# Kernel tuning notes

Measured on AMD Instinct MI355X. Metric: run time of the kernel, lower is better.

The kernel has to match this reference:

```python
import jax, jax.numpy as jnp
import numpy as np

B, OBS, ACT, NT, E, H1, H2, D = 4096, 390, 20, 10, 8, 1024, 512, 256


def setup_inputs() -> dict:
    key = jax.random.key(0)
    ks = jax.random.split(key, 16)
    f32 = jnp.float32

    def w(k, shape, fan_in):
        return jax.random.normal(k, shape, f32) / np.float32(np.sqrt(fan_in))

    return {
        "state_feat": jax.random.normal(ks[0], (B, OBS), f32),
        "act": jax.random.normal(ks[1], (B, ACT), f32),
        "task_id": jax.random.randint(ks[2], (B,), 0, NT, jnp.int32),
        "rep_W1": w(ks[3], (OBS + ACT, H1), OBS + ACT),
        "rep_b1": jnp.zeros((H1,), f32),
        "rep_W2": w(ks[4], (H1, H1), H1),
        "rep_b2": jnp.zeros((H1,), f32),
        "emb": 0.5 * jax.random.normal(ks[5], (NT, D), f32),
        "kW1": w(ks[6], (E, H1, H2), H1),
        "kb1": jnp.zeros((E, H2), f32),
        "kW2": w(ks[7], (E, H2, D), H2),
        "kb2": jnp.zeros((E, D), f32),
        "vW1": w(ks[8], (E, H1, H2), H1),
        "vb1": jnp.zeros((E, H2), f32),
        "vW2": w(ks[9], (E, H2, D), H2),
        "vb2": jnp.zeros((E, D), f32),
        "tW1": w(ks[10], (D, D), D),
        "tb1": jnp.zeros((D,), f32),
        "tW2": w(ks[11], (D, D), D),
        "tb2": jnp.zeros((D,), f32),
        "tW3": w(ks[12], (D, 1), D),
        "tb3": jnp.zeros((1,), f32),
    }


def reference(state_feat, act, task_id, rep_W1, rep_b1, rep_W2, rep_b2, emb,
              kW1, kb1, kW2, kb2, vW1, vb1, vW2, vb2,
              tW1, tb1, tW2, tb2, tW3, tb3):
    # representation: mlp([obs+act, 1024, 1024]) -> ReLU on first layer only
    x = jnp.concatenate([state_feat, act], axis=-1)              # [B, 410]
    rep = jnp.maximum(x @ rep_W1 + rep_b1, 0.0) @ rep_W2 + rep_b2  # [B, H1]
    query = jnp.tanh(emb[task_id])                               # [B, D]

    # batched per-expert key/value MLPs (grouped GEMM instead of python loop)
    hk = jnp.maximum(jnp.einsum('bi,eio->ebo', rep, kW1) + kb1[:, None, :], 0.0)
    keys = jnp.einsum('ebo,eod->ebd', hk, kW2) + kb2[:, None, :]   # [E, B, D]
    hv = jnp.maximum(jnp.einsum('bi,eio->ebo', rep, vW1) + vb1[:, None, :], 0.0)
    vals = jnp.einsum('ebo,eod->ebd', hv, vW2) + vb2[:, None, :]   # [E, B, D]

    scores = jnp.einsum('bd,ebd->be', query, keys)               # [B, E]
    weight = jax.nn.softmax(scores, axis=1)                      # [B, E]
    tower_in = jnp.einsum('be,ebd->bd', weight, vals)            # [B, D]

    # tower: mlp([256, 256, 256, 1]) -> ReLU, ReLU, Identity
    h = jnp.maximum(tower_in @ tW1 + tb1, 0.0)
    h = jnp.maximum(h @ tW2 + tb2, 0.0)
    q = (h @ tW3 + tb3)[:, 0]                                    # [B]

    expert_loss = -jnp.mean(
        jnp.sum(jnp.clip(jnp.log(weight + 1e-10), -6.0, 0.0), axis=-1) * 0.3)
    return q, expert_loss
```

## Files before the change

### kernel.cpp

```cpp
#include <hip/hip_runtime.h>

constexpr int Bn   = 4096;
constexpr int OBS  = 390;
constexpr int ACTN = 20;
constexpr int IN   = 410;
constexpr int KPAD = 448;
constexpr int E    = 8;
constexpr int NT   = 10;
constexpr int H1   = 1024;
constexpr int H2   = 512;
constexpr int D    = 256;

typedef __bf16 bf16x8 __attribute__((ext_vector_type(8)));
typedef float  f32x4  __attribute__((ext_vector_type(4)));
typedef unsigned short u16x8 __attribute__((ext_vector_type(8)));

__device__ __forceinline__ unsigned short f2bf(float f) {
    unsigned int u = __float_as_uint(f);
    unsigned int r = u + 0x7fffu + ((u >> 16) & 1u);
    return (unsigned short)(r >> 16);
}
__device__ __forceinline__ float bf2f(unsigned short h) {
    return __uint_as_float(((unsigned int)h) << 16);
}
__device__ __forceinline__ void gload16(void* lds_dst, const void* g_src) {
    __builtin_amdgcn_global_load_lds(
        (const __attribute__((address_space(1))) void*)g_src,
        (__attribute__((address_space(3))) void*)lds_dst,
        16, 0, 0);
}

struct TD2 {
    const float* W;
    unsigned short* WT;
    int K, Kpad, N;
    long long gsW, gsO;
    int tilesN, perG, start;
};
struct TD2Arr { TD2 d[8]; };

constexpr int PREPB = (Bn * KPAD) / 256;

__global__ __launch_bounds__(256) void prep_all(
    TD2Arr da, int tcb,
    const float* __restrict__ sf, const float* __restrict__ ac,
    unsigned short* __restrict__ x,
    const float* __restrict__ kW2, const float* __restrict__ kb2,
    const float* __restrict__ emb, float* __restrict__ qp, float* __restrict__ qb,
    const float* __restrict__ kb1, const float* __restrict__ vb1,
    float* __restrict__ b1cat)
{
    __shared__ float tile[64][68];
    int bid = blockIdx.x;
    int t = threadIdx.x;

    if (bid < tcb) {
        int i = 0;
#pragma unroll
        for (int j = 1; j < 8; ++j) if (bid >= da.d[j].start) i = j;
        TD2 dd = da.d[i];
        int local = bid - dd.start;
        int g   = local / dd.perG;
        int rem = local - g * dd.perG;
        int kt  = rem / dd.tilesN;
        int nt  = rem - kt * dd.tilesN;
        const float* W = dd.W + (long long)g * dd.gsW;
        unsigned short* WT = dd.WT + (long long)g * dd.gsO;
        int k0 = kt * 64, n0 = nt * 64;
        {
            int kl  = t >> 4;
            int nl4 = (t & 15) * 4;
#pragma unroll
            for (int r = 0; r < 4; ++r) {
                int k = k0 + kl + r * 16;
                float4 v = make_float4(0.f, 0.f, 0.f, 0.f);
                if (k < dd.K) v = *(const float4*)(W + (long long)k * dd.N + n0 + nl4);
                *(float4*)&tile[kl + r * 16][nl4] = v;
            }
        }
        __syncthreads();
        int nl = t >> 2, kc = (t & 3) * 16;
        if (k0 + kc < dd.Kpad) {
            u16x8 o0, o1;
#pragma unroll
            for (int j = 0; j < 8; ++j) {
                o0[j] = f2bf(tile[kc + j][nl]);
                o1[j] = f2bf(tile[kc + 8 + j][nl]);
            }
            unsigned short* dst = WT + (long long)(n0 + nl) * dd.Kpad + k0 + kc;
            *(u16x8*)dst       = o0;
            *(u16x8*)(dst + 8) = o1;
        }
        return;
    }
    int bid2 = bid - tcb;
    if (bid2 < PREPB) {
        int idx = bid2 * 256 + t;
        int b = idx / KPAD;
        int k = idx - b * KPAD;
        float v = 0.f;
        if (k < OBS) v = sf[b * OBS + k];
        else if (k < IN) v = ac[b * ACTN + (k - OBS)];
        x[idx] = f2bf(v);
        return;
    }
    if (bid2 < PREPB + 17) {
        int qbid = bid2 - PREPB;
        float* tq = &tile[0][0];
        for (int i = t; i < NT * D; i += 256) tq[i] = tanhf(emb[i]);
        __syncthreads();
        if (qbid < 16) {
            int e = qbid >> 1;
            int h = (qbid & 1) * 256 + t;
            const float4* row = (const float4*)(kW2 + ((long long)e * H2 + h) * D);
            float acc[NT] = {};
            for (int d4 = 0; d4 < D / 4; ++d4) {
                float4 wv = row[d4];
#pragma unroll
                for (int tt = 0; tt < NT; ++tt)
                    acc[tt] += wv.x * tq[tt * D + d4 * 4] + wv.y * tq[tt * D + d4 * 4 + 1]
                             + wv.z * tq[tt * D + d4 * 4 + 2] + wv.w * tq[tt * D + d4 * 4 + 3];
            }
#pragma unroll
            for (int tt = 0; tt < NT; ++tt)
                qp[((long long)e * NT + tt) * H2 + h] = acc[tt];
        } else if (t < E * NT) {
            int e = t / NT, tt = t - e * NT;
            float s = 0.f;
            for (int d = 0; d < D; ++d) s += kb2[e * D + d] * tq[tt * D + d];
            qb[e * NT + tt] = s;
        }
        return;
    }
    int i = (bid2 - PREPB - 17) * 256 + t;
    b1cat[i] = (i < E * H2) ? kb1[i] : vb1[i - E * H2];
}

template <int KT, int ACTF, int OUTF>
__global__ __launch_bounds__(256, 3) void gemm64x128(
    const unsigned short* __restrict__ A, const unsigned short* __restrict__ BT,
    const float* __restrict__ bias, void* __restrict__ Cout,
    int ldc, long long gsA, long long gsBT, long long gsBias, long long gsC,
    const float* __restrict__ tW3 = nullptr, float* __restrict__ qpart = nullptr)
{
    constexpr int NTK = KT / 64;
    static_assert(NTK >= 2, "KT must be >= 128");

    const int g = blockIdx.z;
    A    += (long long)g * gsA;
    BT   += (long long)g * gsBT;
    bias += (long long)g * gsBias;
    float*          Cf = (float*)Cout + (long long)g * gsC;
    unsigned short* Cb = (unsigned short*)Cout + (long long)g * gsC;

    __shared__ __align__(16) char smem[49152];
    const int tid = threadIdx.x;
    const int l  = tid & 63, lr = l & 15, lk = l >> 4;
    const int w  = tid >> 6;
    const int gm = blockIdx.y * 64, gn = blockIdx.x * 128;

    const int srow = tid >> 3;
    const int cg   = (tid & 7) ^ (srow & 7);
    const unsigned short* gA = A  + (long long)(gm + srow) * KT + cg * 8;
    const unsigned short* gB = BT + (long long)(gn + srow) * KT + cg * 8;
    const int wb = w * 1024;

    const int cs0 = ((0 | lk) ^ (lr & 7)) * 16;
    const int cs1 = ((4 | lk) ^ (lr & 7)) * 16;
    const int aRow = lr * 128;
    const int bRow = 8192 + (w * 32 + lr) * 128;

    f32x4 acc[4][2] = {};

    auto stA = [&](int c, int kt) {
#pragma unroll
        for (int j = 0; j < 2; ++j)
            gload16(smem + c * 24576 + j * 4096 + wb,
                    gA + (long long)(j * 32) * KT + kt * 64);
    };
    auto stB = [&](int c, int kt) {
#pragma unroll
        for (int j = 0; j < 4; ++j)
            gload16(smem + c * 24576 + 8192 + j * 4096 + wb,
                    gB + (long long)(j * 32) * KT + kt * 64);
    };

    stA(0, 0); stB(0, 0); stA(1, 1); stB(1, 1);
    asm volatile("s_waitcnt vmcnt(6)" ::: "memory");
    __builtin_amdgcn_s_barrier();
    __builtin_amdgcn_sched_barrier(0);

#pragma unroll
    for (int kt = 0; kt < NTK; ++kt) {
        const int c = kt & 1;
        const char* bufc = smem + c * 24576;
        bf16x8 a[4][2], b[1][2], b2[1][2];

#pragma unroll
        for (int m = 0; m < 4; ++m) {
            const char* base = bufc + aRow + m * 2048;
            a[m][0] = *(const bf16x8*)(base + cs0);
            a[m][1] = *(const bf16x8*)(base + cs1);
        }
        {
            const char* base = bufc + bRow;
            b[0][0] = *(const bf16x8*)(base + cs0);
            b[0][1] = *(const bf16x8*)(base + cs1);
        }
        __builtin_amdgcn_s_setprio(1);
#pragma unroll
        for (int ks = 0; ks < 2; ++ks)
#pragma unroll
            for (int m = 0; m < 4; ++m)
                acc[m][0] = __builtin_amdgcn_mfma_f32_16x16x32_bf16(
                    a[m][ks], b[0][ks], acc[m][0], 0, 0, 0);
        __builtin_amdgcn_s_setprio(0);

        {
            const char* base = bufc + bRow + 2048;
            b2[0][0] = *(const bf16x8*)(base + cs0);
            b2[0][1] = *(const bf16x8*)(base + cs1);
        }
        asm volatile("s_waitcnt lgkmcnt(0)" ::: "memory");
        __builtin_amdgcn_sched_barrier(0);
        if (kt + 2 < NTK) {
            __builtin_amdgcn_s_barrier();
            __builtin_amdgcn_sched_barrier(0);
            stA(c, kt + 2); stB(c, kt + 2);
        }
        __builtin_amdgcn_s_setprio(1);
#pragma unroll
        for (int ks = 0; ks < 2; ++ks)
#pragma unroll
            for (int m = 0; m < 4; ++m)
                acc[m][1] = __builtin_amdgcn_mfma_f32_16x16x32_bf16(
                    a[m][ks], b2[0][ks], acc[m][1], 0, 0, 0);
        __builtin_amdgcn_s_setprio(0);

        if (kt + 1 < NTK) {
            if (kt + 2 < NTK) { asm volatile("s_waitcnt vmcnt(6)" ::: "memory"); }
            else              { asm volatile("s_waitcnt vmcnt(0)" ::: "memory"); }
            __builtin_amdgcn_sched_barrier(0);
            __builtin_amdgcn_s_barrier();
            __builtin_amdgcn_sched_barrier(0);
        }
    }

    const int orow0 = gm + lk * 4;
    const int ocol0 = gn + w * 32 + lr;
    float bv[2];
#pragma unroll
    for (int nf = 0; nf < 2; ++nf) bv[nf] = bias[gn + w * 32 + lr + nf * 16];

    if (OUTF == 2) {
        float tw3v[2];
#pragma unroll
        for (int nf = 0; nf < 2; ++nf) tw3v[nf] = tW3[gn + w * 32 + lr + nf * 16];
#pragma unroll
        for (int mi = 0; mi < 4; ++mi)
#pragma unroll
            for (int r = 0; r < 4; ++r) {
                float part = 0.f;
#pragma unroll
                for (int nf = 0; nf < 2; ++nf) {
                    float v = acc[mi][nf][r] + bv[nf];
                    if (ACTF == 1) v = fmaxf(v, 0.f);
                    part += v * tw3v[nf];
                }
                part += __shfl_xor(part, 1);
                part += __shfl_xor(part, 2);
                part += __shfl_xor(part, 4);
                part += __shfl_xor(part, 8);
                if (lr == 0)
                    qpart[(orow0 + mi * 16 + r) * 8 + blockIdx.x * 4 + w] = part;
            }
    } else {
#pragma unroll
        for (int mi = 0; mi < 4; ++mi)
#pragma unroll
            for (int nf = 0; nf < 2; ++nf)
#pragma unroll
                for (int r = 0; r < 4; ++r) {
                    float v = acc[mi][nf][r] + bv[nf];
                    if (ACTF == 1) v = fmaxf(v, 0.f);
                    long long off = (long long)(orow0 + mi * 16 + r) * ldc + ocol0 + nf * 16;
                    if (OUTF == 0) Cf[off] = v;
                    else           Cb[off] = f2bf(v);
                }
    }
}

template <int KTOT, int ACTF, int OUTF, int SC>
__global__ __launch_bounds__(512, 2) void gemm256(
    const unsigned short* __restrict__ A, const unsigned short* __restrict__ BT,
    const float* __restrict__ bias, void* __restrict__ Cout,
    int ldc, long long gsA, long long gsBT, long long gsBias, long long gsC,
    const int* __restrict__ task_id, const float* __restrict__ qp,
    float* __restrict__ spart)
{
    constexpr int NT_ = KTOT / 64;
    static_assert(NT_ >= 4 && (NT_ % 2) == 0, "KTOT must be multiple of 128");

    const int g = blockIdx.z;
    A    += (long long)g * gsA;
    BT   += (long long)g * gsBT;
    bias += (long long)g * gsBias;
    float*          Cf = (float*)Cout + (long long)g * gsC;
    unsigned short* Cb = (unsigned short*)Cout + (long long)g * gsC;

    __shared__ __align__(16) char smem[131072];

    const int tid = threadIdx.x;
    const int l  = tid & 63;
    const int lr = l & 15, lk = l >> 4;
    const int w  = tid >> 6;
    const int wr = w >> 2, wc = w & 3;
    const int gm = blockIdx.y * 256, gn = blockIdx.x * 256;

    const int srow = tid >> 3;
    const int cg   = (tid & 7) ^ (srow & 7);
    const unsigned short* gA = A  + (long long)(gm + srow) * KTOT + cg * 8;
    const unsigned short* gB = BT + (long long)(gn + srow) * KTOT + cg * 8;
    const int wbase = (tid & ~63) * 16;

    const int cs0 = ((0 | lk) ^ (lr & 7)) * 16;
    const int cs1 = ((4 | lk) ^ (lr & 7)) * 16;
    const int aRow = wr * 16384 + lr * 128;
    const int bRow = 32768 + (wc >> 1) * 16384 + ((wc & 1) * 64 + lr) * 128;

    f32x4 acc[8][4] = {};

    auto stA = [&](int c, int s, int kt) {
        const unsigned short* src = gA + (long long)(s * 128) * KTOT + kt * 64;
        char* d = smem + c * 65536 + s * 16384 + wbase;
        gload16(d,        src);
        gload16(d + 8192, src + (long long)64 * KTOT);
    };
    auto stB = [&](int c, int s, int kt) {
        const unsigned short* src = gB + (long long)(s * 128) * KTOT + kt * 64;
        char* d = smem + c * 65536 + 32768 + s * 16384 + wbase;
        gload16(d,        src);
        gload16(d + 8192, src + (long long)64 * KTOT);
    };

    stA(0, 0, 0); stA(0, 1, 0); stB(0, 0, 0); stB(0, 1, 0);
    stA(1, 0, 1); stA(1, 1, 1); stB(1, 0, 1); stB(1, 1, 1);
    asm volatile("s_waitcnt vmcnt(8)" ::: "memory");
    __builtin_amdgcn_s_barrier();
    __builtin_amdgcn_sched_barrier(0);

#pragma unroll
    for (int kt = 0; kt < NT_; ++kt) {
        const int c = kt & 1;
        const char* bufc = smem + c * 65536;
        bf16x8 a0[4], a1[4], b0[4], b1[4];

#pragma unroll
        for (int m = 0; m < 4; ++m) {
            const char* base = bufc + aRow + m * (16 * 128);
            a0[m] = *(const bf16x8*)(base + cs0);
            a1[m] = *(const bf16x8*)(base + cs1);
        }
#pragma unroll
        for (int n = 0; n < 4; ++n) {
            const char* base = bufc + bRow + n * (16 * 128);
            b0[n] = *(const bf16x8*)(base + cs0);
            b1[n] = *(const bf16x8*)(base + cs1);
        }
        __builtin_amdgcn_s_setprio(1);
#pragma unroll
        for (int m = 0; m < 4; ++m)
#pragma unroll
            for (int n = 0; n < 4; ++n) {
                acc[m][n] = __builtin_amdgcn_mfma_f32_16x16x32_bf16(a0[m], b0[n], acc[m][n], 0, 0, 0);
                acc[m][n] = __builtin_amdgcn_mfma_f32_16x16x32_bf16(a1[m], b1[n], acc[m][n], 0, 0, 0);
            }
        __builtin_amdgcn_s_setprio(0);

#pragma unroll
        for (int m = 0; m < 4; ++m) {
            const char* base = bufc + aRow + (64 + m * 16) * 128;
            a0[m] = *(const bf16x8*)(base + cs0);
            a1[m] = *(const bf16x8*)(base + cs1);
        }
        asm volatile("s_waitcnt lgkmcnt(0)" ::: "memory");
        __builtin_amdgcn_sched_barrier(0);
        if (kt + 2 < NT_) {
            __builtin_amdgcn_s_barrier();
            __builtin_amdgcn_sched_barrier(0);
            stA(c, 0, kt + 2); stA(c, 1, kt + 2);
            stB(c, 0, kt + 2); stB(c, 1, kt + 2);
        }
        __builtin_amdgcn_s_setprio(1);
#pragma unroll
        for (int m = 0; m < 4; ++m)
#pragma unroll
            for (int n = 0; n < 4; ++n) {
                acc[4 + m][n] = __builtin_amdgcn_mfma_f32_16x16x32_bf16(a0[m], b0[n], acc[4 + m][n], 0, 0, 0);
                acc[4 + m][n] = __builtin_amdgcn_mfma_f32_16x16x32_bf16(a1[m], b1[n], acc[4 + m][n], 0, 0, 0);
            }
        __builtin_amdgcn_s_setprio(0);

        if (kt + 1 < NT_) {
            if (kt + 2 < NT_) { asm volatile("s_waitcnt vmcnt(8)" ::: "memory"); }
            else              { asm volatile("s_waitcnt vmcnt(0)" ::: "memory"); }
            __builtin_amdgcn_sched_barrier(0);
            __builtin_amdgcn_s_barrier();
            __builtin_amdgcn_sched_barrier(0);
        }
    }

    const int orow0 = gm + wr * 128 + lk * 4;
    const int ocol0 = gn + wc * 64 + lr;
    float bv[4];
#pragma unroll
    for (int ni = 0; ni < 4; ++ni) bv[ni] = bias[gn + wc * 64 + lr + ni * 16];

    if (SC && g < E) {
        __syncthreads();
        float* qpl  = (float*)smem;
        int*   tidl = (int*)(smem + NT * 256 * 4);
        for (int i = tid; i < NT * 256; i += 512) {
            int tt = i >> 8, cc = i & 255;
            qpl[i] = qp[((long long)(g * NT + tt)) * H2 + gn + cc];
        }
        if (tid < 256) tidl[tid] = task_id[gm + tid];
        __syncthreads();

        const int rbase = wr * 128 + lk * 4;
        const int cbase = wc * 64 + lr;
#pragma unroll
        for (int mi = 0; mi < 8; ++mi) {
#pragma unroll
            for (int r = 0; r < 4; ++r) {
                int trow = tidl[rbase + mi * 16 + r];
                float rp = 0.f;
#pragma unroll
                for (int ni = 0; ni < 4; ++ni) {
                    float v = acc[mi][ni][r] + bv[ni];
                    v = fmaxf(v, 0.f);
                    rp += v * qpl[trow * 256 + cbase + ni * 16];
                }
                rp += __shfl_xor(rp, 1);
                rp += __shfl_xor(rp, 2);
                rp += __shfl_xor(rp, 4);
                rp += __shfl_xor(rp, 8);
                if (lr == 0)
                    spart[(((long long)g * Bn + orow0 + mi * 16 + r) << 3)
                          + (wc << 1) + blockIdx.x] = rp;
            }
        }
    } else {
#pragma unroll
        for (int mi = 0; mi < 8; ++mi)
#pragma unroll
            for (int ni = 0; ni < 4; ++ni)
#pragma unroll
                for (int r = 0; r < 4; ++r) {
                    float v = acc[mi][ni][r] + bv[ni];
                    if (ACTF == 1) v = fmaxf(v, 0.f);
                    long long off = (long long)(orow0 + mi * 16 + r) * ldc + ocol0 + ni * 16;
                    if (OUTF == 0) Cf[off] = v;
                    else           Cb[off] = f2bf(v);
                }
    }
}

__global__ __launch_bounds__(256) void attn_kernel(
    const float* __restrict__ spart, const float* __restrict__ qb,
    const int* __restrict__ task_id, const unsigned short* __restrict__ vals,
    unsigned short* __restrict__ tower_in, float* __restrict__ loss_partial)
{
    int wv   = threadIdx.x >> 6;
    int lane = threadIdx.x & 63;
    int b    = blockIdx.x * 4 + wv;
    int t    = task_id[b];

    float s[E];
#pragma unroll
    for (int e = 0; e < E; ++e) {
        const float4* sp = (const float4*)(spart + (((long long)e * Bn + b) << 3));
        float4 p0 = sp[0], p1 = sp[1];
        s[e] = p0.x + p0.y + p0.z + p0.w + p1.x + p1.y + p1.z + p1.w + qb[e * NT + t];
    }

    float m = s[0];
#pragma unroll
    for (int e = 1; e < E; ++e) m = fmaxf(m, s[e]);
    float wgt[E];
    float sum = 0.f;
#pragma unroll
    for (int e = 0; e < E; ++e) { wgt[e] = expf(s[e] - m); sum += wgt[e]; }
    float inv = 1.f / sum;

    int d0 = lane * 4;
    float4 acc = make_float4(0.f, 0.f, 0.f, 0.f);
    float lb = 0.f;
#pragma unroll
    for (int e = 0; e < E; ++e) {
        float we = wgt[e] * inv;
        uint2 vv = *(const uint2*)&vals[((long long)e * Bn + b) * D + d0];
        acc.x += we * __uint_as_float(vv.x << 16);
        acc.y += we * __uint_as_float(vv.x & 0xffff0000u);
        acc.z += we * __uint_as_float(vv.y << 16);
        acc.w += we * __uint_as_float(vv.y & 0xffff0000u);
        lb += fminf(fmaxf(logf(we + 1e-10f), -6.f), 0.f);
    }
    ushort4 o;
    o.x = f2bf(acc.x); o.y = f2bf(acc.y); o.z = f2bf(acc.z); o.w = f2bf(acc.w);
    *(ushort4*)&tower_in[(long long)b * D + d0] = o;

    __shared__ float sm[4];
    if (lane == 0) sm[wv] = lb;
    __syncthreads();
    if (threadIdx.x == 0)
        loss_partial[blockIdx.x] = sm[0] + sm[1] + sm[2] + sm[3];
}

__global__ __launch_bounds__(256) void qfin_kernel(
    const float* __restrict__ qpart, const float* __restrict__ tb3,
    float* __restrict__ out, const float* __restrict__ lossp)
{
    if (blockIdx.x == Bn / 256) {
        float s = 0.f;
        for (int i = threadIdx.x; i < Bn / 4; i += 256) s += lossp[i];
#pragma unroll
        for (int off = 32; off > 0; off >>= 1) s += __shfl_xor(s, off, 64);
        __shared__ float sm[4];
        if ((threadIdx.x & 63) == 0) sm[threadIdx.x >> 6] = s;
        __syncthreads();
        if (threadIdx.x == 0) out[Bn] = (-0.3f / Bn) * (sm[0] + sm[1] + sm[2] + sm[3]);
        return;
    }
    int b = blockIdx.x * 256 + threadIdx.x;
    const float4* qq = (const float4*)&qpart[b * 8];
    float4 a0 = qq[0], a1 = qq[1];
    out[b] = a0.x + a0.y + a0.z + a0.w + a1.x + a1.y + a1.z + a1.w + tb3[0];
}

extern "C" void kernel_launch(void* const* d_in, const int* in_sizes, int n_in,
                              void* d_out, int out_size, void* d_ws, size_t ws_size,
                              hipStream_t stream) {
    const float* state_feat = (const float*)d_in[0];
    const float* act        = (const float*)d_in[1];
    const int*   task_id    = (const int*)d_in[2];
    const float* rep_W1 = (const float*)d_in[3];
    const float* rep_b1 = (const float*)d_in[4];
    const float* rep_W2 = (const float*)d_in[5];
    const float* rep_b2 = (const float*)d_in[6];
    const float* emb    = (const float*)d_in[7];
    const float* kW1 = (const float*)d_in[8];
    const float* kb1 = (const float*)d_in[9];
    const float* kW2 = (const float*)d_in[10];
    const float* kb2 = (const float*)d_in[11];
    const float* vW1 = (const float*)d_in[12];
    const float* vb1 = (const float*)d_in[13];
    const float* vW2 = (const float*)d_in[14];
    const float* vb2 = (const float*)d_in[15];
    const float* tW1 = (const float*)d_in[16];
    const float* tb1 = (const float*)d_in[17];
    const float* tW2 = (const float*)d_in[18];
    const float* tb2 = (const float*)d_in[19];
    const float* tW3 = (const float*)d_in[20];
    const float* tb3 = (const float*)d_in[21];
    float* out = (float*)d_out;

    char* p = (char*)d_ws;
    auto alloc = [&](size_t bytes) {
        char* r = p;
        p += (bytes + 255) & ~(size_t)255;
        return r;
    };
    unsigned short* x      = (unsigned short*)alloc((size_t)Bn * KPAD * 2);
    unsigned short* repW1T = (unsigned short*)alloc((size_t)H1 * KPAD * 2);
    unsigned short* repW2T = (unsigned short*)alloc((size_t)H1 * H1 * 2);
    unsigned short* w1T    = (unsigned short*)alloc((size_t)2 * E * H2 * H1 * 2);
    unsigned short* w2T    = (unsigned short*)alloc((size_t)E * D * H2 * 2);
    unsigned short* tW1T   = (unsigned short*)alloc((size_t)D * D * 2);
    unsigned short* tW2T   = (unsigned short*)alloc((size_t)D * D * 2);
    float*          b1cat  = (float*)alloc((size_t)2 * E * H2 * 4);
    float*          qp     = (float*)alloc((size_t)E * NT * H2 * 4);
    float*          qb     = (float*)alloc((size_t)E * NT * 4);
    char*           h1zone = alloc((size_t)Bn * H1 * 2);
    unsigned short* rep    = (unsigned short*)alloc((size_t)Bn * H1 * 2);
    unsigned short* hkv    = (unsigned short*)alloc((size_t)2 * E * Bn * H2 * 2);
    unsigned short* vals   = (unsigned short*)alloc((size_t)E * Bn * D * 2);
    float*          spart  = (float*)alloc((size_t)E * Bn * 8 * 4);
    float*          qpart  = (float*)alloc((size_t)Bn * 8 * 4);
    float*          lossp  = (float*)alloc((size_t)(Bn / 4) * 4);

    unsigned short* h1       = (unsigned short*)h1zone;
    unsigned short* tower_in = (unsigned short*)h1zone;
    unsigned short* t1       = (unsigned short*)(h1zone + (size_t)Bn * D * 2);
    unsigned short* hv = hkv + (size_t)E * Bn * H2;

    TD2Arr da;
    int startAcc = 0;
    auto setd = [&](int i, const float* W, unsigned short* WT, int K, int Kpad, int N,
                    long long gsW, long long gsO, int groups) {
        TD2& dd = da.d[i];
        dd.W = W; dd.WT = WT; dd.K = K; dd.Kpad = Kpad; dd.N = N;
        dd.gsW = gsW; dd.gsO = gsO;
        dd.tilesN = N / 64;
        dd.perG = ((Kpad + 63) / 64) * dd.tilesN;
        dd.start = startAcc;
        startAcc += dd.perG * groups;
    };
    setd(0, rep_W1, repW1T, IN, KPAD, H1, 0, 0, 1);
    setd(1, rep_W2, repW2T, H1, H1, H1, 0, 0, 1);
    setd(2, kW1, w1T,                       H1, H1, H2, (long long)H1 * H2, (long long)H2 * H1, E);
    setd(3, vW1, w1T + (size_t)E * H2 * H1, H1, H1, H2, (long long)H1 * H2, (long long)H2 * H1, E);
    setd(4, vW2, w2T,                       H2, H2, D, (long long)H2 * D, (long long)D * H2, E);
    setd(5, tW1, tW1T, D, D, D, 0, 0, 1);
    setd(6, tW2, tW2T, D, D, D, 0, 0, 1);
    da.d[7] = da.d[6];
    da.d[7].start = 0x7fffffff;
    int totalBlocks = startAcc + PREPB + 17 + 32;
    prep_all<<<totalBlocks, 256, 0, stream>>>(
        da, startAcc, state_feat, act, x, kW2, kb2, emb, qp, qb, kb1, vb1, b1cat);

    gemm64x128<KPAD, 1, 1><<<dim3(H1 / 128, Bn / 64, 1), 256, 0, stream>>>(
        x, repW1T, rep_b1, h1, H1, 0, 0, 0, 0);
    gemm64x128<H1, 0, 1><<<dim3(H1 / 128, Bn / 64, 1), 256, 0, stream>>>(
        h1, repW2T, rep_b2, rep, H1, 0, 0, 0, 0);

    gemm256<H1, 1, 1, 1><<<dim3(H2 / 256, Bn / 256, 2 * E), 512, 0, stream>>>(
        rep, w1T, b1cat, hkv, H2,
        0, (long long)H2 * H1, H2, (long long)Bn * H2,
        task_id, qp, spart);
    gemm64x128<H2, 0, 1><<<dim3(D / 128, Bn / 64, E), 256, 0, stream>>>(
        hv, w2T, vb2, vals, D,
        (long long)Bn * H2, (long long)D * H2, D, (long long)Bn * D);

    attn_kernel<<<Bn / 4, 256, 0, stream>>>(
        spart, qb, task_id, vals, tower_in, lossp);

    gemm64x128<D, 1, 1><<<dim3(D / 128, Bn / 64, 1), 256, 0, stream>>>(
        tower_in, tW1T, tb1, t1, D, 0, 0, 0, 0);
    gemm64x128<D, 1, 2><<<dim3(D / 128, Bn / 64, 1), 256, 0, stream>>>(
        t1, tW2T, tb2, nullptr, D, 0, 0, 0, 0, tW3, qpart);

    qfin_kernel<<<Bn / 256 + 1, 256, 0, stream>>>(qpart, tb3, out, lossp);
}
```

Baseline: 160.0 us.

## Retile expert GEMM to 256x128 with smaller LDS, vectorize input prep

The grouped expert GEMM moves from 256x256 tiles with 128KB of LDS to 256x128 tiles with a K-step of 32 and 48KB of LDS. This allows four blocks per CU and doubles the grid, and the B-tile load is issued one stage earlier to overlap with MFMA. The 64x128 GEMM gets the same early B-load schedule. Input concatenation now converts eight elements per thread with vector stores. The trade-off is more A-tile reloads across N blocks and lower MFMA reuse per LDS read.

```diff
diff --git a/kernel.cpp b/kernel.cpp
--- a/kernel.cpp
+++ b/kernel.cpp
@@ -20,9 +20,6 @@
     unsigned int r = u + 0x7fffu + ((u >> 16) & 1u);
     return (unsigned short)(r >> 16);
 }
-__device__ __forceinline__ float bf2f(unsigned short h) {
-    return __uint_as_float(((unsigned int)h) << 16);
-}
 __device__ __forceinline__ void gload16(void* lds_dst, const void* g_src) {
     __builtin_amdgcn_global_load_lds(
         (const __attribute__((address_space(1))) void*)g_src,
@@ -39,7 +36,8 @@
 };
 struct TD2Arr { TD2 d[8]; };
 
-constexpr int PREPB = (Bn * KPAD) / 256;
+constexpr int XCH    = KPAD / 8;
+constexpr int PREPB  = (Bn * XCH) / 256;
 
 __global__ __launch_bounds__(256) void prep_all(
     TD2Arr da, int tcb,
@@ -95,13 +93,30 @@
     }
     int bid2 = bid - tcb;
     if (bid2 < PREPB) {
-        int idx = bid2 * 256 + t;
-        int b = idx / KPAD;
-        int k = idx - b * KPAD;
-        float v = 0.f;
-        if (k < OBS) v = sf[b * OBS + k];
-        else if (k < IN) v = ac[b * ACTN + (k - OBS)];
-        x[idx] = f2bf(v);
+        int cidx = bid2 * 256 + t;
+        int b  = cidx / XCH;
+        int cc = cidx - b * XCH;
+        int k0 = cc * 8;
+        u16x8 o;
+        if (cc < 48) {
+            const float* s = sf + (long long)b * OBS + k0;
+#pragma unroll
+            for (int j = 0; j < 4; ++j) {
+                float2 v = *(const float2*)(s + j * 2);
+                o[j * 2]     = f2bf(v.x);
+                o[j * 2 + 1] = f2bf(v.y);
+            }
+        } else {
+#pragma unroll
+            for (int j = 0; j < 8; ++j) {
+                int k = k0 + j;
+                float v = 0.f;
+                if (k < OBS) v = sf[(long long)b * OBS + k];
+                else if (k < IN) v = ac[b * ACTN + (k - OBS)];
+                o[j] = f2bf(v);
+            }
+        }
+        *(u16x8*)(x + (long long)b * KPAD + k0) = o;
         return;
     }
     if (bid2 < PREPB + 17) {
@@ -185,8 +200,8 @@
                     gB + (long long)(j * 32) * KT + kt * 64);
     };
 
-    stA(0, 0); stB(0, 0); stA(1, 1); stB(1, 1);
-    asm volatile("s_waitcnt vmcnt(6)" ::: "memory");
+    stA(0, 0); stB(0, 0); stA(1, 1);
+    asm volatile("s_waitcnt vmcnt(2)" ::: "memory");
     __builtin_amdgcn_s_barrier();
     __builtin_amdgcn_sched_barrier(0);
 
@@ -207,6 +222,7 @@
             b[0][0] = *(const bf16x8*)(base + cs0);
             b[0][1] = *(const bf16x8*)(base + cs1);
         }
+        if (kt + 1 < NTK) stB(c ^ 1, kt + 1);
         __builtin_amdgcn_s_setprio(1);
 #pragma unroll
         for (int ks = 0; ks < 2; ++ks)
@@ -226,7 +242,7 @@
         if (kt + 2 < NTK) {
             __builtin_amdgcn_s_barrier();
             __builtin_amdgcn_sched_barrier(0);
-            stA(c, kt + 2); stB(c, kt + 2);
+            stA(c, kt + 2);
         }
         __builtin_amdgcn_s_setprio(1);
 #pragma unroll
@@ -238,7 +254,7 @@
         __builtin_amdgcn_s_setprio(0);
 
         if (kt + 1 < NTK) {
-            if (kt + 2 < NTK) { asm volatile("s_waitcnt vmcnt(6)" ::: "memory"); }
+            if (kt + 2 < NTK) { asm volatile("s_waitcnt vmcnt(2)" ::: "memory"); }
             else              { asm volatile("s_waitcnt vmcnt(0)" ::: "memory"); }
             __builtin_amdgcn_sched_barrier(0);
             __builtin_amdgcn_s_barrier();
@@ -291,15 +307,15 @@
 }
 
 template <int KTOT, int ACTF, int OUTF, int SC>
-__global__ __launch_bounds__(512, 2) void gemm256(
+__global__ __launch_bounds__(512, 4) void gemm256(
     const unsigned short* __restrict__ A, const unsigned short* __restrict__ BT,
     const float* __restrict__ bias, void* __restrict__ Cout,
     int ldc, long long gsA, long long gsBT, long long gsBias, long long gsC,
     const int* __restrict__ task_id, const float* __restrict__ qp,
     float* __restrict__ spart)
 {
-    constexpr int NT_ = KTOT / 64;
-    static_assert(NT_ >= 4 && (NT_ % 2) == 0, "KTOT must be multiple of 128");
+    constexpr int NTK = KTOT / 32;
+    static_assert(NTK >= 2, "KTOT must be >= 64");
 
     const int g = blockIdx.z;
     A    += (long long)g * gsA;
@@ -308,101 +324,87 @@
     float*          Cf = (float*)Cout + (long long)g * gsC;
     unsigned short* Cb = (unsigned short*)Cout + (long long)g * gsC;
 
-    __shared__ __align__(16) char smem[131072];
+    __shared__ __align__(16) char smem[49152];
 
     const int tid = threadIdx.x;
     const int l  = tid & 63;
     const int lr = l & 15, lk = l >> 4;
     const int w  = tid >> 6;
-    const int wr = w >> 2, wc = w & 3;
-    const int gm = blockIdx.y * 256, gn = blockIdx.x * 256;
-
-    const int srow = tid >> 3;
-    const int cg   = (tid & 7) ^ (srow & 7);
-    const unsigned short* gA = A  + (long long)(gm + srow) * KTOT + cg * 8;
-    const unsigned short* gB = BT + (long long)(gn + srow) * KTOT + cg * 8;
-    const int wbase = (tid & ~63) * 16;
-
-    const int cs0 = ((0 | lk) ^ (lr & 7)) * 16;
-    const int cs1 = ((4 | lk) ^ (lr & 7)) * 16;
-    const int aRow = wr * 16384 + lr * 128;
-    const int bRow = 32768 + (wc >> 1) * 16384 + ((wc & 1) * 64 + lr) * 128;
-
-    f32x4 acc[8][4] = {};
-
-    auto stA = [&](int c, int s, int kt) {
-        const unsigned short* src = gA + (long long)(s * 128) * KTOT + kt * 64;
-        char* d = smem + c * 65536 + s * 16384 + wbase;
-        gload16(d,        src);
-        gload16(d + 8192, src + (long long)64 * KTOT);
+    const int wr = w >> 1, wc = w & 1;
+    const int gm = blockIdx.y * 256, gn = blockIdx.x * 128;
+
+    const int srow = tid >> 2;
+    const int scg  = (tid & 3) ^ ((srow ^ (srow >> 2)) & 3);
+    const unsigned short* gA = A  + (long long)(gm + srow) * KTOT + scg * 8;
+    const unsigned short* gB = BT + (long long)(gn + srow) * KTOT + scg * 8;
+    const int wb = w * 1024;
+
+    const int fsw = (lr ^ (lr >> 2)) & 3;
+    const int csA = (lk ^ fsw) * 16;
+    const int aRowB = (wr * 64 + lr) * 64;
+    const int bRowB = 16384 + (wc * 64 + lr) * 64;
+
+    f32x4 acc[4][4] = {};
+
+    auto stA = [&](int c, int kt) {
+#pragma unroll
+        for (int j = 0; j < 2; ++j)
+            gload16(smem + c * 24576 + j * 8192 + wb,
+                    gA + (long long)(j * 128) * KTOT + kt * 32);
     };
-    auto stB = [&](int c, int s, int kt) {
-        const unsigned short* src = gB + (long long)(s * 128) * KTOT + kt * 64;
-        char* d = smem + c * 65536 + 32768 + s * 16384 + wbase;
-        gload16(d,        src);
-        gload16(d + 8192, src + (long long)64 * KTOT);
+    auto stB = [&](int c, int kt) {
+        gload16(smem + c * 24576 + 16384 + wb,
+                gB + kt * 32);
     };
 
-    stA(0, 0, 0); stA(0, 1, 0); stB(0, 0, 0); stB(0, 1, 0);
-    stA(1, 0, 1); stA(1, 1, 1); stB(1, 0, 1); stB(1, 1, 1);
-    asm volatile("s_waitcnt vmcnt(8)" ::: "memory");
+    stA(0, 0); stB(0, 0); stA(1, 1);
+    asm volatile("s_waitcnt vmcnt(2)" ::: "memory");
     __builtin_amdgcn_s_barrier();
     __builtin_amdgcn_sched_barrier(0);
 
-#pragma unroll
-    for (int kt = 0; kt < NT_; ++kt) {
+#pragma unroll 2
+    for (int kt = 0; kt < NTK; ++kt) {
         const int c = kt & 1;
-        const char* bufc = smem + c * 65536;
-        bf16x8 a0[4], a1[4], b0[4], b1[4];
-
-#pragma unroll
-        for (int m = 0; m < 4; ++m) {
-            const char* base = bufc + aRow + m * (16 * 128);
-            a0[m] = *(const bf16x8*)(base + cs0);
-            a1[m] = *(const bf16x8*)(base + cs1);
-        }
-#pragma unroll
-        for (int n = 0; n < 4; ++n) {
-            const char* base = bufc + bRow + n * (16 * 128);
-            b0[n] = *(const bf16x8*)(base + cs0);
-            b1[n] = *(const bf16x8*)(base + cs1);
-        }
+        const char* bufc = smem + c * 24576;
+        bf16x8 a[4], b[2], b2[2];
+
+#pragma unroll
+        for (int mi = 0; mi < 4; ++mi)
+            a[mi] = *(const bf16x8*)(bufc + aRowB + mi * 1024 + csA);
+#pragma unroll
+        for (int ni = 0; ni < 2; ++ni)
+            b[ni] = *(const bf16x8*)(bufc + bRowB + ni * 1024 + csA);
+        if (kt + 1 < NTK) stB(c ^ 1, kt + 1);
         __builtin_amdgcn_s_setprio(1);
 #pragma unroll
-        for (int m = 0; m < 4; ++m)
-#pragma unroll
-            for (int n = 0; n < 4; ++n) {
-                acc[m][n] = __builtin_amdgcn_mfma_f32_16x16x32_bf16(a0[m], b0[n], acc[m][n], 0, 0, 0);
-                acc[m][n] = __builtin_amdgcn_mfma_f32_16x16x32_bf16(a1[m], b1[n], acc[m][n], 0, 0, 0);
-            }
+        for (int mi = 0; mi < 4; ++mi)
+#pragma unroll
+            for (int ni = 0; ni < 2; ++ni)
+                acc[mi][ni] = __builtin_amdgcn_mfma_f32_16x16x32_bf16(
+                    a[mi], b[ni], acc[mi][ni], 0, 0, 0);
         __builtin_amdgcn_s_setprio(0);
 
 #pragma unroll
-        for (int m = 0; m < 4; ++m) {
-            const char* base = bufc + aRow + (64 + m * 16) * 128;
-            a0[m] = *(const bf16x8*)(base + cs0);
-            a1[m] = *(const bf16x8*)(base + cs1);
-        }
+        for (int ni = 0; ni < 2; ++ni)
+            b2[ni] = *(const bf16x8*)(bufc + bRowB + (2 + ni) * 1024 + csA);
         asm volatile("s_waitcnt lgkmcnt(0)" ::: "memory");
         __builtin_amdgcn_sched_barrier(0);
-        if (kt + 2 < NT_) {
+        if (kt + 2 < NTK) {
             __builtin_amdgcn_s_barrier();
             __builtin_amdgcn_sched_barrier(0);
-            stA(c, 0, kt + 2); stA(c, 1, kt + 2);
-            stB(c, 0, kt + 2); stB(c, 1, kt + 2);
+            stA(c, kt + 2);
         }
         __builtin_amdgcn_s_setprio(1);
 #pragma unroll
-        for (int m = 0; m < 4; ++m)
-#pragma unroll
-            for (int n = 0; n < 4; ++n) {
-                acc[4 + m][n] = __builtin_amdgcn_mfma_f32_16x16x32_bf16(a0[m], b0[n], acc[4 + m][n], 0, 0, 0);
-                acc[4 + m][n] = __builtin_amdgcn_mfma_f32_16x16x32_bf16(a1[m], b1[n], acc[4 + m][n], 0, 0, 0);
-            }
+        for (int mi = 0; mi < 4; ++mi)
+#pragma unroll
+            for (int ni = 0; ni < 2; ++ni)
+                acc[mi][2 + ni] = __builtin_amdgcn_mfma_f32_16x16x32_bf16(
+                    a[mi], b2[ni], acc[mi][2 + ni], 0, 0, 0);
         __builtin_amdgcn_s_setprio(0);
 
-        if (kt + 1 < NT_) {
-            if (kt + 2 < NT_) { asm volatile("s_waitcnt vmcnt(8)" ::: "memory"); }
+        if (kt + 1 < NTK) {
+            if (kt + 2 < NTK) { asm volatile("s_waitcnt vmcnt(2)" ::: "memory"); }
             else              { asm volatile("s_waitcnt vmcnt(0)" ::: "memory"); }
             __builtin_amdgcn_sched_barrier(0);
             __builtin_amdgcn_s_barrier();
@@ -410,7 +412,7 @@
         }
     }
 
-    const int orow0 = gm + wr * 128 + lk * 4;
+    const int orow0 = gm + wr * 64 + lk * 4;
     const int ocol0 = gn + wc * 64 + lr;
     float bv[4];
 #pragma unroll
@@ -419,18 +421,18 @@
     if (SC && g < E) {
         __syncthreads();
         float* qpl  = (float*)smem;
-        int*   tidl = (int*)(smem + NT * 256 * 4);
-        for (int i = tid; i < NT * 256; i += 512) {
-            int tt = i >> 8, cc = i & 255;
+        int*   tidl = (int*)(smem + NT * 128 * 4);
+        for (int i = tid; i < NT * 128; i += 512) {
+            int tt = i >> 7, cc = i & 127;
             qpl[i] = qp[((long long)(g * NT + tt)) * H2 + gn + cc];
         }
         if (tid < 256) tidl[tid] = task_id[gm + tid];
         __syncthreads();
 
-        const int rbase = wr * 128 + lk * 4;
+        const int rbase = wr * 64 + lk * 4;
         const int cbase = wc * 64 + lr;
 #pragma unroll
-        for (int mi = 0; mi < 8; ++mi) {
+        for (int mi = 0; mi < 4; ++mi) {
 #pragma unroll
             for (int r = 0; r < 4; ++r) {
                 int trow = tidl[rbase + mi * 16 + r];
@@ -439,7 +441,7 @@
                 for (int ni = 0; ni < 4; ++ni) {
                     float v = acc[mi][ni][r] + bv[ni];
                     v = fmaxf(v, 0.f);
-                    rp += v * qpl[trow * 256 + cbase + ni * 16];
+                    rp += v * qpl[trow * 128 + cbase + ni * 16];
                 }
                 rp += __shfl_xor(rp, 1);
                 rp += __shfl_xor(rp, 2);
@@ -447,12 +449,12 @@
                 rp += __shfl_xor(rp, 8);
                 if (lr == 0)
                     spart[(((long long)g * Bn + orow0 + mi * 16 + r) << 3)
-                          + (wc << 1) + blockIdx.x] = rp;
+                          + (blockIdx.x << 1) + wc] = rp;
             }
         }
     } else {
 #pragma unroll
-        for (int mi = 0; mi < 8; ++mi)
+        for (int mi = 0; mi < 4; ++mi)
 #pragma unroll
             for (int ni = 0; ni < 4; ++ni)
 #pragma unroll
@@ -624,7 +626,7 @@
     gemm64x128<H1, 0, 1><<<dim3(H1 / 128, Bn / 64, 1), 256, 0, stream>>>(
         h1, repW2T, rep_b2, rep, H1, 0, 0, 0, 0);
 
-    gemm256<H1, 1, 1, 1><<<dim3(H2 / 256, Bn / 256, 2 * E), 512, 0, stream>>>(
+    gemm256<H1, 1, 1, 1><<<dim3(H2 / 128, Bn / 256, 2 * E), 512, 0, stream>>>(
         rep, w1T, b1cat, hkv, H2,
         0, (long long)H2 * H1, H2, (long long)Bn * H2,
         task_id, qp, spart);
```

After: 163.5 us. 1.02x slower.

## Issue B-tile loads one stage later, vectorize input prep, prefetch score-epilogue operands

Applied to the files above, without the earlier changes.

In both GEMM kernels the B operand for step kt+1 is now loaded into the other buffer at step kt, right after that buffer's fragments are read, instead of two steps ahead. The vmcnt waits shrink to match. The big GEMM also fills the epilogue's qp/task_id staging into the unused LDS buffer during the last K iteration, which removes a global-load-and-sync round trip before the score reduction. The input-packing prep now writes 8 bf16 values per thread with vector stores instead of one scalar per thread. The later B prefetch gives less latency slack, and writing LDS during the final iteration depends on the buffer-parity reasoning being correct.

```diff
diff --git a/kernel.cpp b/kernel.cpp
--- a/kernel.cpp
+++ b/kernel.cpp
@@ -20,9 +20,6 @@
     unsigned int r = u + 0x7fffu + ((u >> 16) & 1u);
     return (unsigned short)(r >> 16);
 }
-__device__ __forceinline__ float bf2f(unsigned short h) {
-    return __uint_as_float(((unsigned int)h) << 16);
-}
 __device__ __forceinline__ void gload16(void* lds_dst, const void* g_src) {
     __builtin_amdgcn_global_load_lds(
         (const __attribute__((address_space(1))) void*)g_src,
@@ -39,7 +36,8 @@
 };
 struct TD2Arr { TD2 d[8]; };
 
-constexpr int PREPB = (Bn * KPAD) / 256;
+constexpr int XCH    = KPAD / 8;
+constexpr int PREPB  = (Bn * XCH) / 256;
 
 __global__ __launch_bounds__(256) void prep_all(
     TD2Arr da, int tcb,
@@ -95,13 +93,30 @@
     }
     int bid2 = bid - tcb;
     if (bid2 < PREPB) {
-        int idx = bid2 * 256 + t;
-        int b = idx / KPAD;
-        int k = idx - b * KPAD;
-        float v = 0.f;
-        if (k < OBS) v = sf[b * OBS + k];
-        else if (k < IN) v = ac[b * ACTN + (k - OBS)];
-        x[idx] = f2bf(v);
+        int cidx = bid2 * 256 + t;
+        int b  = cidx / XCH;
+        int cc = cidx - b * XCH;
+        int k0 = cc * 8;
+        u16x8 o;
+        if (cc < 48) {
+            const float* s = sf + (long long)b * OBS + k0;
+#pragma unroll
+            for (int j = 0; j < 4; ++j) {
+                float2 v = *(const float2*)(s + j * 2);
+                o[j * 2]     = f2bf(v.x);
+                o[j * 2 + 1] = f2bf(v.y);
+            }
+        } else {
+#pragma unroll
+            for (int j = 0; j < 8; ++j) {
+                int k = k0 + j;
+                float v = 0.f;
+                if (k < OBS) v = sf[(long long)b * OBS + k];
+                else if (k < IN) v = ac[b * ACTN + (k - OBS)];
+                o[j] = f2bf(v);
+            }
+        }
+        *(u16x8*)(x + (long long)b * KPAD + k0) = o;
         return;
     }
     if (bid2 < PREPB + 17) {
@@ -185,8 +200,8 @@
                     gB + (long long)(j * 32) * KT + kt * 64);
     };
 
-    stA(0, 0); stB(0, 0); stA(1, 1); stB(1, 1);
-    asm volatile("s_waitcnt vmcnt(6)" ::: "memory");
+    stA(0, 0); stB(0, 0); stA(1, 1);
+    asm volatile("s_waitcnt vmcnt(2)" ::: "memory");
     __builtin_amdgcn_s_barrier();
     __builtin_amdgcn_sched_barrier(0);
 
@@ -207,6 +222,7 @@
             b[0][0] = *(const bf16x8*)(base + cs0);
             b[0][1] = *(const bf16x8*)(base + cs1);
         }
+        if (kt + 1 < NTK) stB(c ^ 1, kt + 1);
         __builtin_amdgcn_s_setprio(1);
 #pragma unroll
         for (int ks = 0; ks < 2; ++ks)
@@ -226,7 +242,7 @@
         if (kt + 2 < NTK) {
             __builtin_amdgcn_s_barrier();
             __builtin_amdgcn_sched_barrier(0);
-            stA(c, kt + 2); stB(c, kt + 2);
+            stA(c, kt + 2);
         }
         __builtin_amdgcn_s_setprio(1);
 #pragma unroll
@@ -238,7 +254,7 @@
         __builtin_amdgcn_s_setprio(0);
 
         if (kt + 1 < NTK) {
-            if (kt + 2 < NTK) { asm volatile("s_waitcnt vmcnt(6)" ::: "memory"); }
+            if (kt + 2 < NTK) { asm volatile("s_waitcnt vmcnt(2)" ::: "memory"); }
             else              { asm volatile("s_waitcnt vmcnt(0)" ::: "memory"); }
             __builtin_amdgcn_sched_barrier(0);
             __builtin_amdgcn_s_barrier();
@@ -300,6 +316,7 @@
 {
     constexpr int NT_ = KTOT / 64;
     static_assert(NT_ >= 4 && (NT_ % 2) == 0, "KTOT must be multiple of 128");
+    constexpr int QBUF = (((NT_ - 1) & 1) ^ 1) * 65536;
 
     const int g = blockIdx.z;
     A    += (long long)g * gsA;
@@ -344,8 +361,8 @@
     };
 
     stA(0, 0, 0); stA(0, 1, 0); stB(0, 0, 0); stB(0, 1, 0);
-    stA(1, 0, 1); stA(1, 1, 1); stB(1, 0, 1); stB(1, 1, 1);
-    asm volatile("s_waitcnt vmcnt(8)" ::: "memory");
+    stA(1, 0, 1); stA(1, 1, 1);
+    asm volatile("s_waitcnt vmcnt(4)" ::: "memory");
     __builtin_amdgcn_s_barrier();
     __builtin_amdgcn_sched_barrier(0);
 
@@ -355,6 +372,16 @@
         const char* bufc = smem + c * 65536;
         bf16x8 a0[4], a1[4], b0[4], b1[4];
 
+        if (SC && kt == NT_ - 1 && g < E) {
+            float* qpl  = (float*)(smem + QBUF);
+            int*   tidl = (int*)(smem + QBUF + NT * 256 * 4);
+            for (int i = tid; i < NT * 256; i += 512) {
+                int tt = i >> 8, cc = i & 255;
+                qpl[i] = qp[((long long)(g * NT + tt)) * H2 + gn + cc];
+            }
+            if (tid < 256) tidl[tid] = task_id[gm + tid];
+        }
+
 #pragma unroll
         for (int m = 0; m < 4; ++m) {
             const char* base = bufc + aRow + m * (16 * 128);
@@ -367,6 +394,7 @@
             b0[n] = *(const bf16x8*)(base + cs0);
             b1[n] = *(const bf16x8*)(base + cs1);
         }
+        if (kt + 1 < NT_) { stB(c ^ 1, 0, kt + 1); stB(c ^ 1, 1, kt + 1); }
         __builtin_amdgcn_s_setprio(1);
 #pragma unroll
         for (int m = 0; m < 4; ++m)
@@ -389,7 +417,6 @@
             __builtin_amdgcn_s_barrier();
             __builtin_amdgcn_sched_barrier(0);
             stA(c, 0, kt + 2); stA(c, 1, kt + 2);
-            stB(c, 0, kt + 2); stB(c, 1, kt + 2);
         }
         __builtin_amdgcn_s_setprio(1);
 #pragma unroll
@@ -402,7 +429,7 @@
         __builtin_amdgcn_s_setprio(0);
 
         if (kt + 1 < NT_) {
-            if (kt + 2 < NT_) { asm volatile("s_waitcnt vmcnt(8)" ::: "memory"); }
+            if (kt + 2 < NT_) { asm volatile("s_waitcnt vmcnt(4)" ::: "memory"); }
             else              { asm volatile("s_waitcnt vmcnt(0)" ::: "memory"); }
             __builtin_amdgcn_sched_barrier(0);
             __builtin_amdgcn_s_barrier();
@@ -418,14 +445,8 @@
 
     if (SC && g < E) {
         __syncthreads();
-        float* qpl  = (float*)smem;
-        int*   tidl = (int*)(smem + NT * 256 * 4);
-        for (int i = tid; i < NT * 256; i += 512) {
-            int tt = i >> 8, cc = i & 255;
-            qpl[i] = qp[((long long)(g * NT + tt)) * H2 + gn + cc];
-        }
-        if (tid < 256) tidl[tid] = task_id[gm + tid];
-        __syncthreads();
+        const float* qpl  = (const float*)(smem + QBUF);
+        const int*   tidl = (const int*)(smem + QBUF + NT * 256 * 4);
 
         const int rbase = wr * 128 + lk * 4;
         const int cbase = wc * 64 + lr;
```

New measurement: 156.0 us. 1.03x faster.
